# Kernel optimization log

Measured on AMD Instinct MI355X. Metric: run time of the kernel, lower is better.

The kernel has to match this reference:

```python
import jax, jax.numpy as jnp
import numpy as np

B, L = 8, 2048          # images, lines per image
C_IN, HW = 256, 128     # backbone feature channels, spatial size
DIM_LOI = 128
N_PTS0, N_PTS1 = 32, 8  # sampled points per line, after maxpool
SCALE = N_PTS0 // N_PTS1
EPS = 1e-5


def setup_inputs() -> dict:
    key = jax.random.key(0)
    ks = jax.random.split(key, 24)
    d = {}
    d['feature'] = jax.random.normal(ks[0], (B, C_IN, HW, HW), jnp.float32)
    # line endpoints in pixel coords [0, 128)
    d['lines'] = jax.random.uniform(ks[1], (B, L, 2, 2), jnp.float32) * HW
    # fc1: 1x1 conv 256 -> 128
    d['fc1_w'] = jax.random.normal(ks[2], (DIM_LOI, C_IN), jnp.float32) * 0.05
    d['fc1_b'] = jnp.zeros((DIM_LOI,), jnp.float32)
    planes = DIM_LOI // 2
    def bn(k, c):
        k1, k2, k3 = jax.random.split(k, 3)
        return (jax.random.normal(k1, (c,), jnp.float32) * 0.1 + 1.0,
                jax.random.normal(k2, (c,), jnp.float32) * 0.1,
                jax.random.normal(k3, (c,), jnp.float32) * 0.05,
                jax.random.uniform(jax.random.fold_in(k, 7), (c,), jnp.float32, 0.5, 1.5))
    d['bn1_g'], d['bn1_b'], d['bn1_m'], d['bn1_v'] = bn(ks[3], DIM_LOI)
    d['conv1_w'] = jax.random.normal(ks[4], (planes, DIM_LOI), jnp.float32) * 0.05
    d['conv1_b'] = jnp.zeros((planes,), jnp.float32)
    d['bn2_g'], d['bn2_b'], d['bn2_m'], d['bn2_v'] = bn(ks[5], planes)
    d['conv2_w'] = jax.random.normal(ks[6], (planes, planes, 3), jnp.float32) * 0.05
    d['conv2_b'] = jnp.zeros((planes,), jnp.float32)
    d['bn3_g'], d['bn3_b'], d['bn3_m'], d['bn3_v'] = bn(ks[7], planes)
    d['conv3_w'] = jax.random.normal(ks[8], (DIM_LOI, planes), jnp.float32) * 0.05
    d['conv3_b'] = jnp.zeros((DIM_LOI,), jnp.float32)
    d['fc2_w'] = jax.random.normal(ks[9], (1, DIM_LOI * N_PTS1), jnp.float32) * 0.02
    d['fc2_b'] = jnp.zeros((1,), jnp.float32)
    return d


def _bn(x, g, b, m, v):
    # x: [N, C, T], eval-mode batchnorm
    s = g * jax.lax.rsqrt(v + EPS)
    return x * s[None, :, None] + (b - m * s)[None, :, None]


def _loi_forward(feature, lines, fc1_w, fc1_b,
                 bn1_g, bn1_b, bn1_m, bn1_v, conv1_w, conv1_b,
                 bn2_g, bn2_b, bn2_m, bn2_v, conv2_w, conv2_b,
                 bn3_g, bn3_b, bn3_m, bn3_v, conv3_w, conv3_b,
                 fc2_w, fc2_b):
    # fc1: 1x1 conv -> [B, DIM_LOI, H, W]
    x = jnp.einsum('oc,bchw->bohw', fc1_w, feature) + fc1_b[None, :, None, None]

    # sample N_PTS0 points per line: p = p0*lam + p1*(1-lam) - 0.5
    lam = jnp.linspace(0.0, 1.0, N_PTS0, dtype=lines.dtype)  # [P]
    pts = (lines[:, :, 0, None, :] * lam[None, None, :, None]
           + lines[:, :, 1, None, :] * (1.0 - lam[None, None, :, None]) - 0.5)  # [B,L,P,2]
    px, py = pts[..., 0], pts[..., 1]
    px0 = jnp.clip(jnp.floor(px), 0.0, HW - 1.0)
    py0 = jnp.clip(jnp.floor(py), 0.0, HW - 1.0)
    px1 = jnp.clip(px0 + 1.0, 0.0, HW - 1.0)
    py1 = jnp.clip(py0 + 1.0, 0.0, HW - 1.0)
    px0l, py0l = px0.astype(jnp.int32), py0.astype(jnp.int32)
    px1l, py1l = px1.astype(jnp.int32), py1.astype(jnp.int32)

    def gather(f, ix, iy):  # f: [C,H,W], ix/iy: [L,P] -> [C,L,P]
        return f[:, ix, iy]

    gat = jax.vmap(gather)  # over batch
    xp = (gat(x, px0l, py0l) * ((px1 - px) * (py1 - py))[:, None]
          + gat(x, px1l, py0l) * ((px - px0) * (py1 - py))[:, None]
          + gat(x, px0l, py1l) * ((px1 - px) * (py - py0))[:, None]
          + gat(x, px1l, py1l) * ((px - px0) * (py - py0))[:, None])  # [B,C,L,P]

    xp = xp.transpose(0, 2, 1, 3).reshape(B * L, DIM_LOI, N_PTS0)  # [N,C,P]
    # MaxPool1d(kernel=stride=SCALE)
    xp = xp.reshape(B * L, DIM_LOI, N_PTS1, SCALE).max(axis=-1)  # [N,C,T=8]

    # Bottleneck1D residual: x + op(x)
    h = jax.nn.relu(_bn(xp, bn1_g, bn1_b, bn1_m, bn1_v))
    h = jnp.einsum('oc,nct->not', conv1_w, h) + conv1_b[None, :, None]
    h = jax.nn.relu(_bn(h, bn2_g, bn2_b, bn2_m, bn2_v))
    h = jax.lax.conv_general_dilated(h, conv2_w, (1,), [(1, 1)],
                                     dimension_numbers=('NCH', 'OIH', 'NCH'))
    h = h + conv2_b[None, :, None]
    h = jax.nn.relu(_bn(h, bn3_g, bn3_b, bn3_m, bn3_v))
    h = jnp.einsum('oc,nct->not', conv3_w, h) + conv3_b[None, :, None]
    xp = xp + h

    # fc2: ReLU -> Linear(dim_loi*n_pts1, 1)
    flat = jax.nn.relu(xp).reshape(B * L, DIM_LOI * N_PTS1)
    logits = (flat @ fc2_w.T + fc2_b).reshape(-1)  # [B*L]
    return logits


def reference(feature, lines, fc1_w, fc1_b,
              bn1_g, bn1_b, bn1_m, bn1_v, conv1_w, conv1_b,
              bn2_g, bn2_b, bn2_m, bn2_v, conv2_w, conv2_b,
              bn3_g, bn3_b, bn3_m, bn3_v, conv3_w, conv3_b,
              fc2_w, fc2_b):
    return _loi_forward(feature, lines, fc1_w, fc1_b,
                        bn1_g, bn1_b, bn1_m, bn1_v, conv1_w, conv1_b,
                        bn2_g, bn2_b, bn2_m, bn2_v, conv2_w, conv2_b,
                        bn3_g, bn3_b, bn3_m, bn3_v, conv3_w, conv3_b,
                        fc2_w, fc2_b)
```

## Files before the change

kernel.cpp:

```cpp
#include <hip/hip_runtime.h>

#define EPSBN 1e-5f

typedef _Float16 f16;
typedef _Float16 f16x8 __attribute__((ext_vector_type(8)));
typedef _Float16 f16x4 __attribute__((ext_vector_type(4)));
typedef _Float16 f16x2 __attribute__((ext_vector_type(2)));
typedef float    f32x4 __attribute__((ext_vector_type(4)));

#define AS1 __attribute__((address_space(1)))
#define AS3 __attribute__((address_space(3)))

__device__ inline f16x8 hmax8(f16x8 a, f16x8 b) {
    f16x8 r;
    #pragma unroll
    for (int i = 0; i < 8; ++i) r[i] = a[i] > b[i] ? a[i] : b[i];
    return r;
}
__device__ inline f16x8 relu8(f16x8 v) {
    f16x8 r;
    #pragma unroll
    for (int i = 0; i < 8; ++i) r[i] = v[i] > (f16)0.f ? v[i] : (f16)0.f;
    return r;
}

__global__ void wprep_kernel(const float* __restrict__ fc1w,
                             const float* __restrict__ w1,
                             const float* __restrict__ w2,
                             const float* __restrict__ w3,
                             f16* __restrict__ dst) {
    const int i = blockIdx.x * 256 + threadIdx.x;
    float v;
    if (i < 32768) {
        const int k8 = i & 7, otg = (i >> 3) & 7, l = (i >> 6) & 63, s = i >> 12;
        const int n16l = l & 15, quadl = l >> 4;
        v = fc1w[(otg * 16 + n16l) * 256 + s * 32 + quadl * 8 + k8];
    }
    else if (i < 40960) v = w1[i - 32768];
    else if (i < 53248) {
        const int j = i - 40960, tau = j >> 12, rest = j & 4095;
        v = w2[rest * 3 + tau];
    } else              v = w3[i - 53248];
    dst[i] = (f16)v;
}

__global__ __launch_bounds__(1024, 4)
void fc1_mfma(const float* __restrict__ feat,
              const f16*   __restrict__ wfrag,
              const float* __restrict__ bias,
              f16*         __restrict__ xmap) {
    __shared__ f16 wlds[32768];
    __shared__ union {
        float ring[4][4096];
        f16   epi[128][136];
    } u;

    const int tid  = threadIdx.x;
    const int wv   = tid >> 6;
    const int lane = tid & 63;
    const int n16  = lane & 15, quad = lane >> 4;
    const int pw   = wv >> 1;
    const int ow   = wv & 1;
    const int img  = blockIdx.x & 7;
    const int p0   = (blockIdx.x >> 3) << 8;

    const float* fimg = feat + (((size_t)img) << 22);

    f32x4 acc[2][4];
    #pragma unroll
    for (int ptg = 0; ptg < 2; ++ptg)
        #pragma unroll
        for (int t = 0; t < 4; ++t) acc[ptg][t] = (f32x4){0.f, 0.f, 0.f, 0.f};

    const int swz = (wv >> 3) << 2;
    auto issue_hs = [&](int h) {
        const int ch = h * 16 + wv;
        const float* src = fimg + (((size_t)ch) << 14) + p0 + ((lane ^ swz) << 2);
        float* dst = u.ring[h & 3] + (wv << 8);
        __builtin_amdgcn_global_load_lds((const AS1 void*)src,
                                         (AS3 void*)dst, 16, 0, 0);
    };

    #pragma unroll
    for (int c4 = 0; c4 < 4; ++c4) {
        const int c = wv + 16 * c4;
        __builtin_amdgcn_global_load_lds((const AS1 void*)(wfrag + c * 512 + lane * 8),
                                         (AS3 void*)(wlds + c * 512), 16, 0, 0);
    }
    #pragma unroll
    for (int h = 0; h < 4; ++h) issue_hs(h);

    const int xswz = (quad & 1) << 2;

    #pragma unroll
    for (int s = 0; s < 8; ++s) {
        if (s < 7) asm volatile("s_waitcnt vmcnt(2)" ::: "memory");
        else       asm volatile("s_waitcnt vmcnt(0)" ::: "memory");
        __builtin_amdgcn_s_barrier();
        __builtin_amdgcn_sched_barrier(0);

        f16x8 wf[4];
        #pragma unroll
        for (int t = 0; t < 4; ++t)
            wf[t] = *(const f16x8*)&wlds[((s * 64 + lane) * 8 + ow * 4 + t) * 8];

        f16x8 xf[2];
        #pragma unroll
        for (int ptg = 0; ptg < 2; ++ptg) {
            const int pt   = pw * 32 + ptg * 16 + n16;
            const int col  = ((((pt >> 2) ^ xswz) << 2) | (pt & 3));
            const float* fb = u.ring[(2 * s + (quad >> 1)) & 3]
                              + ((quad & 1) << 11) + col;
            f16x8 xv;
            #pragma unroll
            for (int j = 0; j < 8; ++j) xv[j] = (f16)fb[j << 8];
            xf[ptg] = xv;
        }

        #pragma unroll
        for (int ptg = 0; ptg < 2; ++ptg)
            #pragma unroll
            for (int t = 0; t < 4; ++t)
                acc[ptg][t] = __builtin_amdgcn_mfma_f32_16x16x32_f16(wf[t], xf[ptg],
                                                                     acc[ptg][t], 0, 0, 0);

        __builtin_amdgcn_sched_barrier(0);
        __builtin_amdgcn_s_barrier();
        __builtin_amdgcn_sched_barrier(0);
        if (s < 6) { issue_hs(2 * s + 4); issue_hs(2 * s + 5); }
    }

    #pragma unroll
    for (int P = 0; P < 2; ++P) {
        __syncthreads();
        if ((pw >> 2) == P) {
            #pragma unroll
            for (int ptg = 0; ptg < 2; ++ptg) {
                const int rowl = (pw & 3) * 32 + ptg * 16 + n16;
                #pragma unroll
                for (int t = 0; t < 4; ++t) {
                    const int o = ow * 64 + t * 16 + quad * 4;
                    const float4 bq = *(const float4*)&bias[o];
                    f16x4 hv;
                    hv[0] = (f16)(acc[ptg][t][0] + bq.x);
                    hv[1] = (f16)(acc[ptg][t][1] + bq.y);
                    hv[2] = (f16)(acc[ptg][t][2] + bq.z);
                    hv[3] = (f16)(acc[ptg][t][3] + bq.w);
                    *(f16x4*)&u.epi[rowl][o] = hv;
                }
            }
        }
        __syncthreads();
        #pragma unroll
        for (int it = 0; it < 2; ++it) {
            const int idx = it * 1024 + tid;
            const int rowl = idx >> 4, seg = idx & 15;
            const float4 v = *(const float4*)&u.epi[rowl][seg * 8];
            *(float4*)&xmap[(((size_t)(img * 16384 + p0 + P * 128 + rowl)) << 7) + seg * 8] = v;
        }
    }
}

__global__ __launch_bounds__(256)
void loi_kernel(const f16*   __restrict__ x,
                const float* __restrict__ lines,
                const f16*   __restrict__ wsp,
                const float* __restrict__ bn1g, const float* __restrict__ bn1b,
                const float* __restrict__ bn1m, const float* __restrict__ bn1v,
                const float* __restrict__ b1,
                const float* __restrict__ bn2g, const float* __restrict__ bn2b,
                const float* __restrict__ bn2m, const float* __restrict__ bn2v,
                const float* __restrict__ b2,
                const float* __restrict__ bn3g, const float* __restrict__ bn3b,
                const float* __restrict__ bn3m, const float* __restrict__ bn3v,
                const float* __restrict__ b3,
                const float* __restrict__ fc2w, const float* __restrict__ fc2b,
                float* __restrict__ out) {
    __shared__ f16 xp[64][136];
    __shared__ alignas(16) union {
        struct { int toff[256][4]; f16 twgt[256][4]; } tp;
        struct { f16 h1[80][72]; f16 h2[64][72]; } cv;
    } u;
    __shared__ f16 s1h[128], t1h[128];
    __shared__ float s2f[64], t2f[64], s3f[64], t3f[64], b1f[64], b2f[64];
    __shared__ float b3f[128];
    __shared__ float wsum[4][8];

    const f16* w1f16 = wsp + 32768;
    const f16* w2f16 = wsp + 40960;
    const f16* w3f16 = wsp + 53248;

    const int tid  = threadIdx.x;
    const int wv   = tid >> 6, lane = tid & 63;
    const int n16  = lane & 15, quad = lane >> 4;
    const int img  = blockIdx.x & 7;
    const int mblk = blockIdx.x >> 3;

    if (tid < 128) {
        const float s = bn1g[tid] * rsqrtf(bn1v[tid] + EPSBN);
        s1h[tid] = (f16)s; t1h[tid] = (f16)(bn1b[tid] - bn1m[tid] * s);
    }
    if (tid < 64) {
        const float s = bn2g[tid] * rsqrtf(bn2v[tid] + EPSBN);
        s2f[tid] = s; t2f[tid] = bn2b[tid] - bn2m[tid] * s;
        b1f[tid] = b1[tid];
    } else if (tid < 128) {
        const int c = tid - 64;
        const float s = bn3g[c] * rsqrtf(bn3v[c] + EPSBN);
        s3f[c] = s; t3f[c] = bn3b[c] - bn3m[c] * s;
        b2f[c] = b2[c];
    } else {
        b3f[tid - 128] = b3[tid - 128];
    }

    {
        const int li = tid >> 5, pt = tid & 31;
        const int gl = img * 2048 + mblk * 8 + li;
        const float4 ln = *(const float4*)&lines[gl * 4];
        const float lam = (float)pt * (1.0f / 31.0f);
        const float px = ln.x * lam + ln.z * (1.f - lam) - 0.5f;
        const float py = ln.y * lam + ln.w * (1.f - lam) - 0.5f;
        const float px0 = fminf(fmaxf(floorf(px), 0.f), 127.f);
        const float py0 = fminf(fmaxf(floorf(py), 0.f), 127.f);
        const float px1 = fminf(px0 + 1.f, 127.f);
        const float py1 = fminf(py0 + 1.f, 127.f);
        const int ix0 = (int)px0, iy0 = (int)py0;
        const int ix1 = (int)px1, iy1 = (int)py1;
        u.tp.toff[tid][0] = (((ix0 << 7) + iy0) << 7);
        u.tp.toff[tid][1] = (((ix1 << 7) + iy0) << 7);
        u.tp.toff[tid][2] = (((ix0 << 7) + iy1) << 7);
        u.tp.toff[tid][3] = (((ix1 << 7) + iy1) << 7);
        const float wx1 = px1 - px, wx0 = px - px0;
        const float wy1 = py1 - py, wy0 = py - py0;
        u.tp.twgt[tid][0] = (f16)(wx1 * wy1); u.tp.twgt[tid][1] = (f16)(wx0 * wy1);
        u.tp.twgt[tid][2] = (f16)(wx1 * wy0); u.tp.twgt[tid][3] = (f16)(wx0 * wy0);
    }
    __syncthreads();

    {
        const int h  = lane >> 5;
        const int sh = (lane >> 4) & 1;
        const int j  = lane & 15;
        const int li = wv * 2 + h;
        const f16* xbh = x + (((size_t)img) << 21) + 8 * j;
        #pragma unroll
        for (int t = 0; t < 8; ++t) {
            f16x8 m;
            #pragma unroll
            for (int q = 0; q < 8; ++q) m[q] = (f16)(-60000.f);
            #pragma unroll
            for (int ss = 0; ss < 2; ++ss) {
                const int combo = li * 32 + t * 4 + sh * 2 + ss;
                const int4  off = *(const int4*)&u.tp.toff[combo][0];
                const f16x4 tw  = *(const f16x4*)&u.tp.twgt[combo][0];
                const f16x8 g00 = *(const f16x8*)(xbh + off.x);
                const f16x8 g10 = *(const f16x8*)(xbh + off.y);
                const f16x8 g01 = *(const f16x8*)(xbh + off.z);
                const f16x8 g11 = *(const f16x8*)(xbh + off.w);
                f16x8 w0, w1v, w2v, w3v;
                #pragma unroll
                for (int q = 0; q < 8; ++q) {
                    w0[q] = tw[0]; w1v[q] = tw[1]; w2v[q] = tw[2]; w3v[q] = tw[3];
                }
                const f16x8 v = g00 * w0 + g10 * w1v + g01 * w2v + g11 * w3v;
                m = hmax8(m, v);
            }
            union { f16x8 v8; int i4[4]; } cv;
            cv.v8 = m;
            #pragma unroll
            for (int q = 0; q < 4; ++q) cv.i4[q] = __shfl_xor(cv.i4[q], 16, 64);
            m = hmax8(m, cv.v8);
            if (sh == 0) *(f16x8*)&xp[li * 8 + t][8 * j] = m;
        }
    }
    __syncthreads();

    {
        const int r = tid >> 4, seg = tid & 15;
        const int row = (r >> 1) * 10 + (r & 1) * 9;
        *(unsigned long long*)&u.cv.h1[row][seg * 4] = 0ull;
    }

    {
        const int o_lane = wv * 16 + n16;
        f32x4 acc1[4];
        #pragma unroll
        for (int nt = 0; nt < 4; ++nt) acc1[nt] = (f32x4){0.f, 0.f, 0.f, 0.f};
        #pragma unroll
        for (int ks = 0; ks < 4; ++ks) {
            const int k = ks * 32 + quad * 8;
            const f16x8 a  = *(const f16x8*)&w1f16[o_lane * 128 + k];
            const f16x8 s8 = *(const f16x8*)&s1h[k];
            const f16x8 t8 = *(const f16x8*)&t1h[k];
            #pragma unroll
            for (int nt = 0; nt < 4; ++nt) {
                const f16x8 raw = *(const f16x8*)&xp[nt * 16 + n16][k];
                const f16x8 bf = relu8(raw * s8 + t8);
                acc1[nt] = __builtin_amdgcn_mfma_f32_16x16x32_f16(a, bf, acc1[nt], 0, 0, 0);
            }
        }
        #pragma unroll
        for (int nt = 0; nt < 4; ++nt) {
            const int n = nt * 16 + n16;
            const int nprow = (n >> 3) * 10 + (n & 7) + 1;
            #pragma unroll
            for (int r = 0; r < 4; ++r) {
                const int o = wv * 16 + quad * 4 + r;
                const float v = fmaxf((acc1[nt][r] + b1f[o]) * s2f[o] + t2f[o], 0.f);
                u.cv.h1[nprow][o] = (f16)v;
            }
        }
    }
    __syncthreads();

    {
        const int o_lane = wv * 16 + n16;
        f32x4 acc2[4];
        #pragma unroll
        for (int nt = 0; nt < 4; ++nt) acc2[nt] = (f32x4){0.f, 0.f, 0.f, 0.f};
        #pragma unroll
        for (int d = 0; d < 3; ++d) {
            const f16* A2 = w2f16 + d * 4096;
            #pragma unroll
            for (int ks = 0; ks < 2; ++ks) {
                const int k = ks * 32 + quad * 8;
                const f16x8 a = *(const f16x8*)&A2[o_lane * 64 + k];
                #pragma unroll
                for (int nt = 0; nt < 4; ++nt) {
                    const int n = nt * 16 + n16;
                    const int row = (n >> 3) * 10 + (n & 7) + d;
                    const f16x8 bf = *(const f16x8*)&u.cv.h1[row][k];
                    acc2[nt] = __builtin_amdgcn_mfma_f32_16x16x32_f16(a, bf, acc2[nt], 0, 0, 0);
                }
            }
        }
        #pragma unroll
        for (int nt = 0; nt < 4; ++nt) {
            const int n = nt * 16 + n16;
            #pragma unroll
            for (int r = 0; r < 4; ++r) {
                const int o = wv * 16 + quad * 4 + r;
                const float v = fmaxf((acc2[nt][r] + b2f[o]) * s3f[o] + t3f[o], 0.f);
                u.cv.h2[n][o] = (f16)v;
            }
        }
    }
    __syncthreads();

    {
        const int col = n16 & 7, obase = wv * 16 + quad * 4;
        float fcv[2][4];
        #pragma unroll
        for (int h = 0; h < 2; ++h)
            #pragma unroll
            for (int r = 0; r < 4; ++r)
                fcv[h][r] = fc2w[(h * 64 + obase + r) * 8 + col];

        f32x4 acc3[2][4];
        #pragma unroll
        for (int h = 0; h < 2; ++h)
            #pragma unroll
            for (int nt = 0; nt < 4; ++nt) acc3[h][nt] = (f32x4){0.f, 0.f, 0.f, 0.f};
        #pragma unroll
        for (int ks = 0; ks < 2; ++ks) {
            const int k = ks * 32 + quad * 8;
            const f16x8 a0 = *(const f16x8*)&w3f16[(wv * 16 + n16) * 64 + k];
            const f16x8 a1 = *(const f16x8*)&w3f16[(64 + wv * 16 + n16) * 64 + k];
            #pragma unroll
            for (int nt = 0; nt < 4; ++nt) {
                const f16x8 bf = *(const f16x8*)&u.cv.h2[nt * 16 + n16][k];
                acc3[0][nt] = __builtin_amdgcn_mfma_f32_16x16x32_f16(a0, bf, acc3[0][nt], 0, 0, 0);
                acc3[1][nt] = __builtin_amdgcn_mfma_f32_16x16x32_f16(a1, bf, acc3[1][nt], 0, 0, 0);
            }
        }
        float part[4] = {0.f, 0.f, 0.f, 0.f};
        #pragma unroll
        for (int h = 0; h < 2; ++h) {
            const float4 bq = *(const float4*)&b3f[h * 64 + obase];
            const float bqa[4] = {bq.x, bq.y, bq.z, bq.w};
            #pragma unroll
            for (int nt = 0; nt < 4; ++nt) {
                const int n = nt * 16 + n16;
                const f16x4 rx = *(const f16x4*)&xp[n][h * 64 + obase];
                float p = 0.f;
                #pragma unroll
                for (int r = 0; r < 4; ++r) {
                    float v = acc3[h][nt][r] + bqa[r] + (float)rx[r];
                    v = fmaxf(v, 0.f);
                    p += v * fcv[h][r];
                }
                part[nt] += p;
            }
        }
        #pragma unroll
        for (int off_i = 0; off_i < 5; ++off_i) {
            const int off = (int[]){1, 2, 4, 16, 32}[off_i];
            part[0] += __shfl_xor(part[0], off, 64);
            part[1] += __shfl_xor(part[1], off, 64);
            part[2] += __shfl_xor(part[2], off, 64);
            part[3] += __shfl_xor(part[3], off, 64);
        }
        if ((lane & 55) == 0) {
            const int par = (lane >> 3) & 1;
            wsum[wv][0 + par] = part[0];
            wsum[wv][2 + par] = part[1];
            wsum[wv][4 + par] = part[2];
            wsum[wv][6 + par] = part[3];
        }
    }
    __syncthreads();

    if (tid < 8) {
        const float s = wsum[0][tid] + wsum[1][tid] + wsum[2][tid] + wsum[3][tid];
        out[img * 2048 + mblk * 8 + tid] = s + fc2b[0];
    }
}

extern "C" void kernel_launch(void* const* d_in, const int* in_sizes, int n_in,
                              void* d_out, int out_size, void* d_ws, size_t ws_size,
                              hipStream_t stream) {
    const float* feature = (const float*)d_in[0];
    const float* lines   = (const float*)d_in[1];
    const float* fc1_w   = (const float*)d_in[2];
    const float* fc1_b   = (const float*)d_in[3];
    const float* bn1g    = (const float*)d_in[4];
    const float* bn1b    = (const float*)d_in[5];
    const float* bn1m    = (const float*)d_in[6];
    const float* bn1v    = (const float*)d_in[7];
    const float* w1      = (const float*)d_in[8];
    const float* b1      = (const float*)d_in[9];
    const float* bn2g    = (const float*)d_in[10];
    const float* bn2b    = (const float*)d_in[11];
    const float* bn2m    = (const float*)d_in[12];
    const float* bn2v    = (const float*)d_in[13];
    const float* w2      = (const float*)d_in[14];
    const float* b2      = (const float*)d_in[15];
    const float* bn3g    = (const float*)d_in[16];
    const float* bn3b    = (const float*)d_in[17];
    const float* bn3m    = (const float*)d_in[18];
    const float* bn3v    = (const float*)d_in[19];
    const float* w3      = (const float*)d_in[20];
    const float* b3      = (const float*)d_in[21];
    const float* fc2w    = (const float*)d_in[22];
    const float* fc2b    = (const float*)d_in[23];

    f16* xmap = (f16*)d_ws;
    f16* wsp  = (f16*)((char*)d_ws + (size_t)32 * 1024 * 1024);

    wprep_kernel<<<240, 256, 0, stream>>>(fc1_w, w1, w2, w3, wsp);
    fc1_mfma<<<512, 1024, 0, stream>>>(feature, wsp, fc1_b, xmap);
    loi_kernel<<<2048, 256, 0, stream>>>(xmap, lines, wsp,
                                         bn1g, bn1b, bn1m, bn1v, b1,
                                         bn2g, bn2b, bn2m, bn2v, b2,
                                         bn3g, bn3b, bn3m, bn3v, b3,
                                         fc2w, fc2b, (float*)d_out);
}
```

Measured before the change: 281.9 us.

## Stage fc1 input via registers with f16 conversion into double-buffered LDS

Replaces the direct global-to-LDS fp32 ring buffer in the fc1 MFMA kernel with register-staged loads that are converted to f16 before being written to a double-buffered LDS tile. This halves the LDS footprint and the LDS read traffic per point, and drops the per-element fp32-to-f16 conversion on the MFMA operand read path. In exchange it costs extra VGPRs for the staging registers and adds LDS writes and conversion work inside the main loop. It also uses a simpler schedule with one barrier per step.

```diff
diff --git a/kernel.cpp b/kernel.cpp
--- a/kernel.cpp
+++ b/kernel.cpp
@@ -51,8 +51,8 @@
               f16*         __restrict__ xmap) {
     __shared__ f16 wlds[32768];
     __shared__ union {
-        float ring[4][4096];
-        f16   epi[128][136];
+        f16 xb[2][32][264];
+        f16 epi[128][132];
     } u;
 
     const int tid  = threadIdx.x;
@@ -66,20 +66,14 @@
 
     const float* fimg = feat + (((size_t)img) << 22);
 
+    const int sch = tid >> 5, sg = tid & 31;
+    const float* sbase = fimg + (((size_t)sch) << 14) + p0 + sg * 8;
+
     f32x4 acc[2][4];
     #pragma unroll
     for (int ptg = 0; ptg < 2; ++ptg)
         #pragma unroll
         for (int t = 0; t < 4; ++t) acc[ptg][t] = (f32x4){0.f, 0.f, 0.f, 0.f};
-
-    const int swz = (wv >> 3) << 2;
-    auto issue_hs = [&](int h) {
-        const int ch = h * 16 + wv;
-        const float* src = fimg + (((size_t)ch) << 14) + p0 + ((lane ^ swz) << 2);
-        float* dst = u.ring[h & 3] + (wv << 8);
-        __builtin_amdgcn_global_load_lds((const AS1 void*)src,
-                                         (AS3 void*)dst, 16, 0, 0);
-    };
 
     #pragma unroll
     for (int c4 = 0; c4 < 4; ++c4) {
@@ -87,17 +81,26 @@
         __builtin_amdgcn_global_load_lds((const AS1 void*)(wfrag + c * 512 + lane * 8),
                                          (AS3 void*)(wlds + c * 512), 16, 0, 0);
     }
-    #pragma unroll
-    for (int h = 0; h < 4; ++h) issue_hs(h);
-
-    const int xswz = (quad & 1) << 2;
+    float4 st[2][2];
+    st[0][0] = *(const float4*)(sbase);
+    st[0][1] = *(const float4*)(sbase + 4);
+    st[1][0] = *(const float4*)(sbase + 524288);
+    st[1][1] = *(const float4*)(sbase + 524292);
+    {
+        f16x8 h;
+        #pragma unroll
+        for (int i = 0; i < 4; ++i) { h[i] = (f16)st[0][0][i]; h[i + 4] = (f16)st[0][1][i]; }
+        *(f16x8*)&u.xb[0][sch][sg * 8] = h;
+    }
+    asm volatile("s_waitcnt vmcnt(0)" ::: "memory");
+    __syncthreads();
 
     #pragma unroll
     for (int s = 0; s < 8; ++s) {
-        if (s < 7) asm volatile("s_waitcnt vmcnt(2)" ::: "memory");
-        else       asm volatile("s_waitcnt vmcnt(0)" ::: "memory");
-        __builtin_amdgcn_s_barrier();
-        __builtin_amdgcn_sched_barrier(0);
+        if (s < 6) {
+            st[s & 1][0] = *(const float4*)(sbase + (size_t)(s + 2) * 524288);
+            st[s & 1][1] = *(const float4*)(sbase + (size_t)(s + 2) * 524288 + 4);
+        }
 
         f16x8 wf[4];
         #pragma unroll
@@ -107,13 +110,10 @@
         f16x8 xf[2];
         #pragma unroll
         for (int ptg = 0; ptg < 2; ++ptg) {
-            const int pt   = pw * 32 + ptg * 16 + n16;
-            const int col  = ((((pt >> 2) ^ xswz) << 2) | (pt & 3));
-            const float* fb = u.ring[(2 * s + (quad >> 1)) & 3]
-                              + ((quad & 1) << 11) + col;
+            const int pt = pw * 32 + ptg * 16 + n16;
             f16x8 xv;
             #pragma unroll
-            for (int j = 0; j < 8; ++j) xv[j] = (f16)fb[j << 8];
+            for (int j = 0; j < 8; ++j) xv[j] = u.xb[s & 1][quad * 8 + j][pt];
             xf[ptg] = xv;
         }
 
@@ -124,10 +124,21 @@
                 acc[ptg][t] = __builtin_amdgcn_mfma_f32_16x16x32_f16(wf[t], xf[ptg],
                                                                      acc[ptg][t], 0, 0, 0);
 
-        __builtin_amdgcn_sched_barrier(0);
-        __builtin_amdgcn_s_barrier();
-        __builtin_amdgcn_sched_barrier(0);
-        if (s < 6) { issue_hs(2 * s + 4); issue_hs(2 * s + 5); }
+        if (s < 7) {
+            f16x8 h;
+            #pragma unroll
+            for (int i = 0; i < 4; ++i) {
+                h[i]     = (f16)st[(s + 1) & 1][0][i];
+                h[i + 4] = (f16)st[(s + 1) & 1][1][i];
+            }
+            *(f16x8*)&u.xb[(s + 1) & 1][sch][sg * 8] = h;
+
+            __builtin_amdgcn_sched_barrier(0);
+            asm volatile("s_waitcnt lgkmcnt(0)" ::: "memory");
+            __builtin_amdgcn_sched_barrier(0);
+            __builtin_amdgcn_s_barrier();
+            __builtin_amdgcn_sched_barrier(0);
+        }
     }
 
     #pragma unroll
```

Result: no change. 283.0 us (+0.4%).
